# Kernel optimization log

Hardware: AMD Instinct MI355X
Metric: run time of the kernel (lower is better)

## Reference

```python
import jax, jax.numpy as jnp
import numpy as np

NEG_BIG = -9e15  # matches torch -9000000000000000.0

def setup_inputs() -> dict:
    key = jax.random.key(0)
    k1, k2, k3, k4 = jax.random.split(key, 4)
    B, N, F_IN, F_OUT = 8, 2048, 128, 64
    x = jax.random.normal(k1, (B, N, F_IN), dtype=jnp.float32)
    adj = jax.random.randint(k2, (B, N, N), 0, 2, dtype=jnp.int32)
    # xavier_uniform-style init for params
    limW = float(np.sqrt(6.0 / (F_IN + F_OUT)))
    W = jax.random.uniform(k3, (F_IN, F_OUT), minval=-limW, maxval=limW, dtype=jnp.float32)
    lima = float(np.sqrt(6.0 / (2 * F_OUT + 1)))
    a = jax.random.uniform(k4, (2 * F_OUT, 1), minval=-lima, maxval=lima, dtype=jnp.float32)
    return {"x": x, "adj": adj, "W": W, "a": a}

def reference(x, adj, W, a):
    # x: [B, N, F_in], adj: [B, N, N], W: [F_in, F_out], a: [2*F_out, 1]
    h = jnp.einsum('bnf,fo->bno', x, W)            # [B, N, F_out]
    F_out = W.shape[1]
    # The repeat/cat construction computes a_input[b,i,j] = [h_i ; h_j], so
    # a_input @ a decomposes into f1_i + f2_j without the O(N^2 * 2F) tensor.
    f1 = h @ a[:F_out, 0]                          # [B, N]
    f2 = h @ a[F_out:, 0]                          # [B, N]
    e = jnp.tanh(f1[:, :, None] + f2[:, None, :])  # [B, N, N]
    att = jnp.where(adj > 0, e, NEG_BIG)
    att = jax.nn.softmax(att, axis=2)              # [B, N, N]
    h_prime = jnp.einsum('bmn,bno->bmo', att, h)   # [B, N, F_out]
    return jax.nn.elu(h_prime)                     # concat=True branch
```

## Files before the change

kernel.cpp:

```cpp
#include <hip/hip_runtime.h>
#include <math.h>

#define BB 8
#define NN 2048
#define FIN 128
#define FOUT 64
#define TI 16
#define TJ 256
#define TJP (TJ + 8)
#define NTILE (NN / TJ)

typedef short bf16x8 __attribute__((ext_vector_type(8)));
typedef float f32x4 __attribute__((ext_vector_type(4)));

__device__ __forceinline__ float exp_tanh(float z) {
    float zc = fminf(fmaxf(z, -15.f), 15.f);
    float u = __expf(zc + zc);
    float tn = (u - 1.f) * __builtin_amdgcn_rcpf(u + 1.f);
    return __expf(tn);
}

__device__ __forceinline__ unsigned short f2bf(float x) {
    union { float f; unsigned u; } v; v.f = x;
    unsigned r = v.u + 0x7FFF + ((v.u >> 16) & 1);
    return (unsigned short)(r >> 16);
}

__global__ __launch_bounds__(256, 2) void gat_k1(const float* __restrict__ x,
                                                 const float* __restrict__ W,
                                                 const float* __restrict__ a,
                                                 unsigned short* __restrict__ ht,
                                                 float* __restrict__ f1,
                                                 float* __restrict__ f2) {
    __shared__ __attribute__((aligned(16))) float Wl[FIN][FOUT];
    __shared__ __attribute__((aligned(16))) float xs[16][FIN];
    int t = threadIdx.x;

    const float4* W4 = (const float4*)W;
    float4* Wl4 = (float4*)&Wl[0][0];
#pragma unroll
    for (int kk = 0; kk < 8; ++kk) Wl4[t + 256 * kk] = W4[t + 256 * kk];

    size_t row0 = (size_t)blockIdx.x * 16;
    const float4* x4 = (const float4*)(x + row0 * FIN);
    float4* xs4 = (float4*)&xs[0][0];
#pragma unroll
    for (int kk = 0; kk < 2; ++kk) xs4[t + 256 * kk] = x4[t + 256 * kk];
    __syncthreads();

    int c = t & 63;
    int rq = t >> 6;
    float acc[4] = {0.f, 0.f, 0.f, 0.f};
#pragma unroll 8
    for (int k = 0; k < FIN; ++k) {
        float wv = Wl[k][c];
        acc[0] = fmaf(xs[rq][k], wv, acc[0]);
        acc[1] = fmaf(xs[rq + 4][k], wv, acc[1]);
        acc[2] = fmaf(xs[rq + 8][k], wv, acc[2]);
        acc[3] = fmaf(xs[rq + 12][k], wv, acc[3]);
    }
    float a1c = a[c], a2c = a[FOUT + c];
#pragma unroll
    for (int m = 0; m < 4; ++m) {
        size_t bn = row0 + rq + 4 * m;
        int b = (int)(bn >> 11);
        int n = (int)(bn & 2047);
        ht[((size_t)b * (NN / 32) + (n >> 5)) * (FOUT * 32) + c * 32 + (n & 31)] =
            f2bf(acc[m]);
        float p1 = acc[m] * a1c;
        float p2 = acc[m] * a2c;
#pragma unroll
        for (int off = 32; off > 0; off >>= 1) {
            p1 += __shfl_down(p1, off, 64);
            p2 += __shfl_down(p2, off, 64);
        }
        if (c == 0) { f1[bn] = p1; f2[bn] = p2; }
    }
}

__global__ __launch_bounds__(256) void gat_k2f(const int* __restrict__ adj,
                                               const unsigned short* __restrict__ ht,
                                               const float* __restrict__ f1,
                                               const float* __restrict__ f2,
                                               float* __restrict__ out) {
    __shared__ __attribute__((aligned(16))) unsigned short pb[TI][TJP];
    __shared__ __attribute__((aligned(16))) float f2s[TJ];
    __shared__ float f1s[TI];
    __shared__ float rsw[TI];

    int t = threadIdx.x;
    int i0 = blockIdx.x * TI;
    int b = blockIdx.y;

    int lane = t & 63;
    int w = t >> 6;
    int mrow = lane & 15;
    int quad = lane >> 4;

    int j4 = t & 63;

    if (t < TI) f1s[t] = f1[(size_t)b * NN + i0 + t];
    __syncthreads();

    float f1r[4];
    float ps[4];
#pragma unroll
    for (int m = 0; m < 4; ++m) {
        f1r[m] = f1s[w + 4 * m];
        ps[m] = 0.f;
    }
    f32x4 acc = {0.f, 0.f, 0.f, 0.f};

    const int* adjrow = adj + (((size_t)b * NN + i0) * NN) + 4 * j4;
    const unsigned short* htb =
        ht + (size_t)b * (NN / 32) * (FOUT * 32)
           + (size_t)(w * 16 + mrow) * 32 + 8 * quad;

    for (int jt = 0; jt < NTILE; ++jt) {
        int j0 = jt * TJ;

        int4 avreg[4];
#pragma unroll
        for (int m = 0; m < 4; ++m)
            avreg[m] = *(const int4*)(adjrow + (size_t)(w + 4 * m) * NN + j0);

        f2s[t] = f2[(size_t)b * NN + j0 + t];
        __syncthreads();

        float4 fv = ((const float4*)f2s)[j4];
#pragma unroll
        for (int m = 0; m < 4; ++m) {
            int4 av = avreg[m];
            float f1i = f1r[m];
            float4 p;
            p.x = (av.x > 0) ? exp_tanh(f1i + fv.x) : 0.f;
            p.y = (av.y > 0) ? exp_tanh(f1i + fv.y) : 0.f;
            p.z = (av.z > 0) ? exp_tanh(f1i + fv.z) : 0.f;
            p.w = (av.w > 0) ? exp_tanh(f1i + fv.w) : 0.f;
            ps[m] += p.x + p.y + p.z + p.w;
            ushort4 pk;
            pk.x = f2bf(p.x); pk.y = f2bf(p.y);
            pk.z = f2bf(p.z); pk.w = f2bf(p.w);
            *(ushort4*)&pb[w + 4 * m][4 * j4] = pk;
        }
        __syncthreads();

        const unsigned short* prow = &pb[mrow][8 * quad];
        const unsigned short* hpan = htb + (size_t)(j0 >> 5) * (FOUT * 32);
#pragma unroll
        for (int ch = 0; ch < TJ / 32; ++ch) {
            bf16x8 af = *(const bf16x8*)(prow + 32 * ch);
            bf16x8 bf = *(const bf16x8*)(hpan + (size_t)ch * (FOUT * 32));
            acc = __builtin_amdgcn_mfma_f32_16x16x32_bf16(af, bf, acc, 0, 0, 0);
        }
    }

#pragma unroll
    for (int m = 0; m < 4; ++m) {
        float s = ps[m];
#pragma unroll
        for (int off = 32; off > 0; off >>= 1) s += __shfl_down(s, off, 64);
        if (lane == 0) rsw[w + 4 * m] = s;
    }
    __syncthreads();

    float* op = out + ((size_t)b * NN + i0) * FOUT + w * 16 + mrow;
#pragma unroll
    for (int u = 0; u < 4; ++u) {
        int row = quad * 4 + u;
        float rinv = __builtin_amdgcn_rcpf(rsw[row]);
        float sx = acc[u] * rinv;
        op[(size_t)row * FOUT] = (sx > 0.f) ? sx : expm1f(sx);
    }
}

extern "C" void kernel_launch(void* const* d_in, const int* in_sizes, int n_in,
                              void* d_out, int out_size, void* d_ws, size_t ws_size,
                              hipStream_t stream) {
    const float* x   = (const float*)d_in[0];
    const int*   adj = (const int*)d_in[1];
    const float* W   = (const float*)d_in[2];
    const float* a   = (const float*)d_in[3];
    float* out = (float*)d_out;

    unsigned short* ht = (unsigned short*)d_ws;
    float* f1   = (float*)(ht + (size_t)BB * FOUT * NN);
    float* f2   = f1 + (size_t)BB * NN;

    gat_k1<<<dim3(BB * NN / 16), dim3(256), 0, stream>>>(x, W, a, ht, f1, f2);
    gat_k2f<<<dim3(NN / TI, BB), dim3(256), 0, stream>>>(adj, ht, f1, f2, out);
}
```

Measured before the change: 216.3 us.

## Double-buffer probability tile and prefetch next adjacency/f2 during MFMA

Each thread now prefetches the next tile's adjacency row chunks and f2 values into registers before running the current tile's MFMA loop, so global load latency overlaps with the matrix work. The probability tile in shared memory is double-buffered, which drops one of the two block barriers per tile. f2 is read directly from global instead of being staged through shared memory. A sched_barrier pins the prefetch ahead of the MFMA loop. The cost is more register pressure and twice the shared memory for the probability buffer.

```diff
diff --git a/kernel.cpp b/kernel.cpp
--- a/kernel.cpp
+++ b/kernel.cpp
@@ -83,8 +83,7 @@
                                                const float* __restrict__ f1,
                                                const float* __restrict__ f2,
                                                float* __restrict__ out) {
-    __shared__ __attribute__((aligned(16))) unsigned short pb[TI][TJP];
-    __shared__ __attribute__((aligned(16))) float f2s[TJ];
+    __shared__ __attribute__((aligned(16))) unsigned short pb[2][TI][TJP];
     __shared__ float f1s[TI];
     __shared__ float rsw[TI];
 
@@ -96,7 +95,6 @@
     int w = t >> 6;
     int mrow = lane & 15;
     int quad = lane >> 4;
-
     int j4 = t & 63;
 
     if (t < TI) f1s[t] = f1[(size_t)b * NN + i0 + t];
@@ -112,40 +110,51 @@
     f32x4 acc = {0.f, 0.f, 0.f, 0.f};
 
     const int* adjrow = adj + (((size_t)b * NN + i0) * NN) + 4 * j4;
+    const float* f2b = f2 + (size_t)b * NN + 4 * j4;
     const unsigned short* htb =
         ht + (size_t)b * (NN / 32) * (FOUT * 32)
            + (size_t)(w * 16 + mrow) * 32 + 8 * quad;
 
+    int4 avreg[4];
+    float4 fv;
+#pragma unroll
+    for (int m = 0; m < 4; ++m)
+        avreg[m] = *(const int4*)(adjrow + (size_t)(w + 4 * m) * NN);
+    fv = *(const float4*)f2b;
+
     for (int jt = 0; jt < NTILE; ++jt) {
         int j0 = jt * TJ;
-
-        int4 avreg[4];
-#pragma unroll
-        for (int m = 0; m < 4; ++m)
-            avreg[m] = *(const int4*)(adjrow + (size_t)(w + 4 * m) * NN + j0);
-
-        f2s[t] = f2[(size_t)b * NN + j0 + t];
-        __syncthreads();
-
-        float4 fv = ((const float4*)f2s)[j4];
+        unsigned short (*pbc)[TJP] = pb[jt & 1];
+
+        float4 f = fv;
 #pragma unroll
         for (int m = 0; m < 4; ++m) {
             int4 av = avreg[m];
             float f1i = f1r[m];
             float4 p;
-            p.x = (av.x > 0) ? exp_tanh(f1i + fv.x) : 0.f;
-            p.y = (av.y > 0) ? exp_tanh(f1i + fv.y) : 0.f;
-            p.z = (av.z > 0) ? exp_tanh(f1i + fv.z) : 0.f;
-            p.w = (av.w > 0) ? exp_tanh(f1i + fv.w) : 0.f;
+            p.x = (av.x > 0) ? exp_tanh(f1i + f.x) : 0.f;
+            p.y = (av.y > 0) ? exp_tanh(f1i + f.y) : 0.f;
+            p.z = (av.z > 0) ? exp_tanh(f1i + f.z) : 0.f;
+            p.w = (av.w > 0) ? exp_tanh(f1i + f.w) : 0.f;
             ps[m] += p.x + p.y + p.z + p.w;
             ushort4 pk;
             pk.x = f2bf(p.x); pk.y = f2bf(p.y);
             pk.z = f2bf(p.z); pk.w = f2bf(p.w);
-            *(ushort4*)&pb[w + 4 * m][4 * j4] = pk;
-        }
+            *(ushort4*)&pbc[w + 4 * m][4 * j4] = pk;
+        }
+
         __syncthreads();
 
-        const unsigned short* prow = &pb[mrow][8 * quad];
+        if (jt + 1 < NTILE) {
+#pragma unroll
+            for (int m = 0; m < 4; ++m)
+                avreg[m] = *(const int4*)(adjrow + (size_t)(w + 4 * m) * NN
+                                          + j0 + TJ);
+            fv = *(const float4*)(f2b + j0 + TJ);
+        }
+        __builtin_amdgcn_sched_barrier(0);
+
+        const unsigned short* prow = &pbc[mrow][8 * quad];
         const unsigned short* hpan = htb + (size_t)(j0 >> 5) * (FOUT * 32);
 #pragma unroll
         for (int ch = 0; ch < TJ / 32; ++ch) {
```

New measurement: 218.3 us. Within noise of the previous version (+0.9%).
